# Kernel optimization log

Hardware: AMD Instinct MI355X
Metric: run time of the kernel (lower is better)

The kernel has to match this reference:

```python
import jax, jax.numpy as jnp
import numpy as np

B, N, IN_DIM = 16, 768, 16
HID, EMB, N_LAYERS, N_HEADS = 64, 128, 2, 8


def setup_inputs() -> dict:
    key = jax.random.key(0)
    ks = jax.random.split(key, 10)
    s = lambda fan_in: 1.0 / np.sqrt(fan_in)
    inp = {
        "x": jax.random.normal(ks[0], (B, N, IN_DIM), dtype=jnp.float32),
        "ip_w": jax.random.uniform(ks[1], (IN_DIM, HID), jnp.float32, -s(IN_DIM), s(IN_DIM)),
        "ip_b": jax.random.uniform(ks[2], (HID,), jnp.float32, -s(IN_DIM), s(IN_DIM)),
        # layer 0: in_features = HID; layer 1: in_features = HID * N_HEADS
        "gat_w0": jax.random.uniform(ks[3], (N_HEADS, HID, HID), jnp.float32, -s(HID), s(HID)),
        "gat_a0": jax.random.uniform(ks[4], (N_HEADS, 2 * HID), jnp.float32, -s(2 * HID), s(2 * HID)),
        "gat_w1": jax.random.uniform(ks[5], (N_HEADS, HID * N_HEADS, HID), jnp.float32, -s(HID * N_HEADS), s(HID * N_HEADS)),
        "gat_a1": jax.random.uniform(ks[6], (N_HEADS, 2 * HID), jnp.float32, -s(2 * HID), s(2 * HID)),
        "proj_w": jax.random.uniform(ks[7], (HID * N_HEADS, EMB), jnp.float32, -s(HID * N_HEADS), s(HID * N_HEADS)),
        "proj_b": jax.random.uniform(ks[8], (EMB,), jnp.float32, -s(HID * N_HEADS), s(HID * N_HEADS)),
    }
    return inp


def _gat_layer(h, W, a):
    # h: [B, N, F_in]; W: [H, F_in, F_out]; a: [H, 2*F_out]
    Wh = jnp.einsum("bnf,hfo->bhno", h, W)  # [B,H,N,F_out]
    f_out = W.shape[-1]
    a1, a2 = a[:, :f_out], a[:, f_out:]
    # additive attention decomposed: e_ij = leakyrelu(a1.Wh_i + a2.Wh_j)
    s1 = jnp.einsum("bhno,ho->bhn", Wh, a1)
    s2 = jnp.einsum("bhno,ho->bhn", Wh, a2)
    e = jax.nn.leaky_relu(s1[..., :, None] + s2[..., None, :], negative_slope=0.2)
    # adj = ones -> mask is a no-op; dense softmax over neighbors
    att = jax.nn.softmax(e, axis=-1)  # [B,H,N,N]
    hp = jnp.einsum("bhnm,bhmo->bhno", att, Wh)
    b, hds, n, f = hp.shape
    return hp.transpose(0, 2, 1, 3).reshape(b, n, hds * f)  # concat heads


def reference(x, ip_w, ip_b, gat_w0, gat_a0, gat_w1, gat_a1, proj_w, proj_b):
    h = x @ ip_w + ip_b  # input_proj
    h = _gat_layer(h, gat_w0, gat_a0)
    h = _gat_layer(h, gat_w1, gat_a1)
    # dropout identity (eval); final activation (ELU) is never applied in forward
    return h @ proj_w + proj_b  # [B, N, EMB]
```

## Files before the change

kernel.cpp:

```cpp
#include <hip/hip_runtime.h>
#include <hip/hip_bf16.h>


#define B_ 16
#define N_ 768
#define IN_DIM_ 16
#define HID_ 64
#define EMB_ 128
#define NH_ 8
#define F1_ (NH_ * HID_)
#define LOG2E_ 1.4426950408889634f

typedef __attribute__((ext_vector_type(4))) float f32x4;
typedef __attribute__((ext_vector_type(8))) short bf16x8;

static __device__ __forceinline__ short f2bf(float x) {
    __hip_bfloat16 b = __float2bfloat16(x);
    return *reinterpret_cast<short*>(&b);
}

__global__ __launch_bounds__(256) void k_h0frag(const float* __restrict__ x,
                                                const float* __restrict__ w,
                                                const float* __restrict__ bias,
                                                ushort* __restrict__ h0A) {
    const int t = blockIdx.x * 256 + threadIdx.x;
    const int lane = t & 63;
    const int kt = (t >> 6) & 1;
    const int rtg = t >> 7;
    const int row = rtg * 16 + (lane & 15);
    const int k0 = kt * 32 + (lane >> 4) * 8;
    const float* xr = x + row * IN_DIM_;
    float xv[IN_DIM_];
#pragma unroll
    for (int f = 0; f < IN_DIM_; ++f) xv[f] = xr[f];
    bf16x8 v;
#pragma unroll
    for (int j = 0; j < 8; ++j) {
        float acc = bias[k0 + j];
#pragma unroll
        for (int f = 0; f < IN_DIM_; ++f) acc = fmaf(xv[f], w[f * HID_ + k0 + j], acc);
        v[j] = f2bf(acc);
    }
    *(bf16x8*)&h0A[t * 8] = v;
}

__global__ __launch_bounds__(256) void k_cvtw(const float* __restrict__ w1,
                                              const float* __restrict__ pw,
                                              const float* __restrict__ w0,
                                              ushort* __restrict__ W1f,
                                              ushort* __restrict__ pwf,
                                              ushort* __restrict__ W0f) {
    int t = blockIdx.x * 256 + threadIdx.x;
    if (t < 32768) {
        int lane = t & 63, nt = (t >> 6) & 3, kt = (t >> 8) & 15, h = t >> 12;
        int k0 = kt * 32 + (lane >> 4) * 8;
        int col = nt * 16 + (lane & 15);
        const float* src = w1 + (h * 512 + k0) * 64 + col;
        bf16x8 v;
#pragma unroll
        for (int j = 0; j < 8; ++j) v[j] = f2bf(src[j * 64]);
        *(bf16x8*)&W1f[t * 8] = v;
    } else if (t < 40960) {
        int u = t - 32768;
        int lane = u & 63, nt = (u >> 6) & 7, kt = u >> 9;
        int k0 = kt * 32 + (lane >> 4) * 8;
        int col = nt * 16 + (lane & 15);
        const float* src = pw + k0 * 128 + col;
        bf16x8 v;
#pragma unroll
        for (int j = 0; j < 8; ++j) v[j] = f2bf(src[j * 128]);
        *(bf16x8*)&pwf[u * 8] = v;
    } else {
        int u = t - 40960;
        int lane = u & 63, nt = (u >> 6) & 3, kt = (u >> 8) & 1, h = u >> 9;
        int k0 = kt * 32 + (lane >> 4) * 8;
        int col = nt * 16 + (lane & 15);
        const float* src = w0 + (h * 64 + k0) * 64 + col;
        bf16x8 v;
#pragma unroll
        for (int j = 0; j < 8; ++j) v[j] = f2bf(src[j * 64]);
        *(bf16x8*)&W0f[u * 8] = v;
    }
}

#define TBSTRIDE 40

__global__ __launch_bounds__(256) void k_wh1m(const ushort* __restrict__ h0A,
                                              const ushort* __restrict__ W0f,
                                              const float* __restrict__ a,
                                              ushort* __restrict__ Whf,
                                              float* __restrict__ s1,
                                              float* __restrict__ s2) {
    __shared__ __align__(16) ushort tb[4][64 * TBSTRIDE];
    const int bid = blockIdx.x;
    const int chunk = bid % 6;
    const int h = (bid / 6) % NH_;
    const int b = bid / (6 * NH_);
    const int bh = b * NH_ + h;

    const int lane = threadIdx.x & 63;
    const int w = threadIdx.x >> 6;
    const int lg = lane >> 4;
    const int ll = lane & 15;

    f32x4 zero4 = {0.f, 0.f, 0.f, 0.f};
    f32x4 acc[2][4];
#pragma unroll
    for (int mt = 0; mt < 2; ++mt)
#pragma unroll
        for (int nt = 0; nt < 4; ++nt) acc[mt][nt] = zero4;

    const int rt0 = b * 48 + chunk * 8 + w * 2;
#pragma unroll
    for (int kt = 0; kt < 2; ++kt) {
        bf16x8 afr[2];
#pragma unroll
        for (int mt = 0; mt < 2; ++mt)
            afr[mt] = *(const bf16x8*)&h0A[(((rt0 + mt) * 2) + kt) * 512 + lane * 8];
        bf16x8 bfr[4];
#pragma unroll
        for (int nt = 0; nt < 4; ++nt)
            bfr[nt] = *(const bf16x8*)&W0f[(((h * 2 + kt) * 4) + nt) * 512 + lane * 8];
#pragma unroll
        for (int mt = 0; mt < 2; ++mt)
#pragma unroll
            for (int nt = 0; nt < 4; ++nt)
                acc[mt][nt] = __builtin_amdgcn_mfma_f32_16x16x32_bf16(afr[mt], bfr[nt], acc[mt][nt], 0, 0, 0);
    }

    float a1v[4], a2v[4];
#pragma unroll
    for (int nt = 0; nt < 4; ++nt) {
        a1v[nt] = a[h * 2 * HID_ + nt * 16 + ll];
        a2v[nt] = a[h * 2 * HID_ + HID_ + nt * 16 + ll];
    }
    const int n0 = chunk * 128;
    float* s1b = s1 + bh * N_ + n0 + w * 32;
    float* s2b = s2 + bh * N_ + n0 + w * 32;
    ushort* tbw = tb[w];
#pragma unroll
    for (int mt = 0; mt < 2; ++mt) {
#pragma unroll
        for (int reg = 0; reg < 4; ++reg) {
            const int r32 = mt * 16 + lg * 4 + reg;
            float p1 = 0.f, p2 = 0.f;
#pragma unroll
            for (int nt = 0; nt < 4; ++nt) {
                float v = acc[mt][nt][reg];
                p1 = fmaf(v, a1v[nt], p1);
                p2 = fmaf(v, a2v[nt], p2);
            }
#pragma unroll
            for (int off = 8; off; off >>= 1) {
                p1 += __shfl_xor(p1, off);
                p2 += __shfl_xor(p2, off);
            }
            if (ll == 0) {
                s1b[r32] = p1;
                s2b[r32] = p2;
            }
#pragma unroll
            for (int nt = 0; nt < 4; ++nt) {
                int c = nt * 16 + ll;
                tbw[c * TBSTRIDE + r32] = (ushort)f2bf(acc[mt][nt][reg]);
            }
        }
    }
    __syncthreads();

    const int kt2 = chunk * 4 + w;
#pragma unroll
    for (int nt = 0; nt < 4; ++nt) {
        int c = nt * 16 + ll;
        bf16x8 v = *(const bf16x8*)&tbw[c * TBSTRIDE + lg * 8];
        *(bf16x8*)&Whf[(bh * 24 + kt2) * 2048 + nt * 512 + lane * 8] = v;
    }
}

__global__ __launch_bounds__(256) void k_attn(const ushort* __restrict__ Whf,
                                              const float* __restrict__ s1,
                                              const float* __restrict__ s2,
                                              ushort* __restrict__ hpA) {
    __shared__ __align__(16) float t1s[128];
    __shared__ __align__(16) float t2s[N_];
    __shared__ __align__(16) float dls[128];
    __shared__ __align__(16) ushort hbuf[128 * 64];
    const int bid = blockIdx.x;
    const int nc = bid % (N_ / 128);
    const int h = (bid / (N_ / 128)) % NH_;
    const int b = bid / ((N_ / 128) * NH_);
    const int n0 = nc * 128;
    const int bh = b * NH_ + h;

    const float* s1g = s1 + bh * N_;
    const float* s2g = s2 + bh * N_;
    for (int i = threadIdx.x; i < N_; i += 256) t2s[i] = s2g[i] * LOG2E_;
    if (threadIdx.x < 128) t1s[threadIdx.x] = s1g[n0 + threadIdx.x] * LOG2E_;
    __syncthreads();

    const int lane = threadIdx.x & 63;
    const int w = threadIdx.x >> 6;
    const int rowbase = w * 32;
    const int lg = lane >> 4;
    const int ll = lane & 15;

    const float t1a = t1s[rowbase + ll];
    const float t1b = t1s[rowbase + 16 + ll];

    f32x4 zero4 = {0.f, 0.f, 0.f, 0.f};
    f32x4 acc[2][4];
    f32x4 dacc[2];
#pragma unroll
    for (int mt = 0; mt < 2; ++mt) {
        dacc[mt] = zero4;
#pragma unroll
        for (int nt = 0; nt < 4; ++nt) acc[mt][nt] = zero4;
    }

    bf16x8 onesB;
#pragma unroll
    for (int j = 0; j < 8; ++j) onesB[j] = (ll == 0) ? (short)0x3F80 : (short)0;

    const ushort* Wbase = Whf + bh * ((N_ / 32) * 2048);

    for (int ktile = 0; ktile < N_ / 32; ++ktile) {
        bf16x8 bq[4];
        const ushort* p = Wbase + ktile * 2048 + lane * 8;
#pragma unroll
        for (int nt = 0; nt < 4; ++nt) bq[nt] = *(const bf16x8*)(p + nt * 512);

        float qv[8];
        const float* q = &t2s[ktile * 32 + lg * 8];
#pragma unroll
        for (int j = 0; j < 8; ++j) qv[j] = q[j];

#pragma unroll
        for (int mt = 0; mt < 2; ++mt) {
            const float t1v = mt ? t1b : t1a;
            bf16x8 af;
#pragma unroll
            for (int j = 0; j < 8; ++j) {
                float e = t1v + qv[j];
                e = fmaxf(e, 0.2f * e);
                af[j] = f2bf(exp2f(e));
            }
            dacc[mt] = __builtin_amdgcn_mfma_f32_16x16x32_bf16(af, onesB, dacc[mt], 0, 0, 0);
#pragma unroll
            for (int nt = 0; nt < 4; ++nt)
                acc[mt][nt] = __builtin_amdgcn_mfma_f32_16x16x32_bf16(af, bq[nt], acc[mt][nt], 0, 0, 0);
        }
    }

#pragma unroll
    for (int mt = 0; mt < 2; ++mt) {
        if (ll == 0) {
#pragma unroll
            for (int reg = 0; reg < 4; ++reg)
                dls[rowbase + mt * 16 + lg * 4 + reg] = dacc[mt][reg];
        }
    }
    __syncthreads();

    char* hb8 = (char*)hbuf;
#pragma unroll
    for (int mt = 0; mt < 2; ++mt) {
#pragma unroll
        for (int reg = 0; reg < 4; ++reg) {
            const int row = rowbase + mt * 16 + lg * 4 + reg;
            const float inv = 1.0f / dls[row];
            const int swz = (row & 7) << 4;
#pragma unroll
            for (int nt = 0; nt < 4; ++nt) {
                int c = nt * 16 + ll;
                *(ushort*)(hb8 + row * 128 + ((c * 2) ^ swz)) =
                    (ushort)f2bf(acc[mt][nt][reg] * inv);
            }
        }
    }
    __syncthreads();

#pragma unroll
    for (int rt2 = 0; rt2 < 2; ++rt2) {
#pragma unroll
        for (int kc = 0; kc < 2; ++kc) {
            const int rtl = w * 2 + rt2;
            const int row = rtl * 16 + ll;
            bf16x8 v = *(const bf16x8*)(hb8 + row * 128 +
                                        (((kc * 64 + lg * 16)) ^ ((row & 7) << 4)));
            const int rtg = b * 48 + nc * 8 + rtl;
            *(bf16x8*)&hpA[((rtg * 16) + (h * 2 + kc)) * 512 + lane * 8] = v;
        }
    }
}

__global__ __launch_bounds__(256) void k_wh2(const ushort* __restrict__ hpA,
                                             const ushort* __restrict__ W1f,
                                             const float* __restrict__ a,
                                             ushort* __restrict__ Whf,
                                             float* __restrict__ s1,
                                             float* __restrict__ s2) {
    __shared__ __align__(16) ushort tb[4][64 * TBSTRIDE];
    const int bid = blockIdx.x;
    const int chunk = bid % 6;
    const int h = (bid / 6) % NH_;
    const int b = bid / (6 * NH_);
    const int bh = b * NH_ + h;

    const int lane = threadIdx.x & 63;
    const int w = threadIdx.x >> 6;
    const int lg = lane >> 4;
    const int ll = lane & 15;

    f32x4 zero4 = {0.f, 0.f, 0.f, 0.f};
    f32x4 acc[2][4];
#pragma unroll
    for (int mt = 0; mt < 2; ++mt)
#pragma unroll
        for (int nt = 0; nt < 4; ++nt) acc[mt][nt] = zero4;

    const int rt0 = b * 48 + chunk * 8 + w * 2;
    for (int kt = 0; kt < 16; ++kt) {
        bf16x8 afr[2];
#pragma unroll
        for (int mt = 0; mt < 2; ++mt)
            afr[mt] = *(const bf16x8*)&hpA[(((rt0 + mt) * 16) + kt) * 512 + lane * 8];
        bf16x8 bfr[4];
#pragma unroll
        for (int nt = 0; nt < 4; ++nt)
            bfr[nt] = *(const bf16x8*)&W1f[(((h * 16 + kt) * 4) + nt) * 512 + lane * 8];
#pragma unroll
        for (int mt = 0; mt < 2; ++mt)
#pragma unroll
            for (int nt = 0; nt < 4; ++nt)
                acc[mt][nt] = __builtin_amdgcn_mfma_f32_16x16x32_bf16(afr[mt], bfr[nt], acc[mt][nt], 0, 0, 0);
    }

    float a1v[4], a2v[4];
#pragma unroll
    for (int nt = 0; nt < 4; ++nt) {
        a1v[nt] = a[h * 2 * HID_ + nt * 16 + ll];
        a2v[nt] = a[h * 2 * HID_ + HID_ + nt * 16 + ll];
    }
    const int n0 = chunk * 128;
    float* s1b = s1 + bh * N_ + n0 + w * 32;
    float* s2b = s2 + bh * N_ + n0 + w * 32;
    ushort* tbw = tb[w];
#pragma unroll
    for (int mt = 0; mt < 2; ++mt) {
#pragma unroll
        for (int reg = 0; reg < 4; ++reg) {
            const int r32 = mt * 16 + lg * 4 + reg;
            float p1 = 0.f, p2 = 0.f;
#pragma unroll
            for (int nt = 0; nt < 4; ++nt) {
                float v = acc[mt][nt][reg];
                p1 = fmaf(v, a1v[nt], p1);
                p2 = fmaf(v, a2v[nt], p2);
            }
#pragma unroll
            for (int off = 8; off; off >>= 1) {
                p1 += __shfl_xor(p1, off);
                p2 += __shfl_xor(p2, off);
            }
            if (ll == 0) {
                s1b[r32] = p1;
                s2b[r32] = p2;
            }
#pragma unroll
            for (int nt = 0; nt < 4; ++nt) {
                int c = nt * 16 + ll;
                tbw[c * TBSTRIDE + r32] = (ushort)f2bf(acc[mt][nt][reg]);
            }
        }
    }
    __syncthreads();

    const int kt2 = chunk * 4 + w;
#pragma unroll
    for (int nt = 0; nt < 4; ++nt) {
        int c = nt * 16 + ll;
        bf16x8 v = *(const bf16x8*)&tbw[c * TBSTRIDE + lg * 8];
        *(bf16x8*)&Whf[(bh * 24 + kt2) * 2048 + nt * 512 + lane * 8] = v;
    }
}

__global__ __launch_bounds__(256) void k_projm(const ushort* __restrict__ hpA,
                                               const ushort* __restrict__ pwf,
                                               const float* __restrict__ bias,
                                               float* __restrict__ out) {
    const int blk = blockIdx.x;
    const int lane = threadIdx.x & 63;
    const int w = threadIdx.x >> 6;
    const int wrow = w >> 1, wcol = w & 1;
    const int lg = lane >> 4;
    const int ll = lane & 15;

    f32x4 zero4 = {0.f, 0.f, 0.f, 0.f};
    f32x4 acc[4];
#pragma unroll
    for (int nt = 0; nt < 4; ++nt) acc[nt] = zero4;

    const int rt = blk * 2 + wrow;
    for (int kt = 0; kt < 16; ++kt) {
        bf16x8 afr = *(const bf16x8*)&hpA[((rt * 16) + kt) * 512 + lane * 8];
        bf16x8 bfr[4];
#pragma unroll
        for (int nt = 0; nt < 4; ++nt)
            bfr[nt] = *(const bf16x8*)&pwf[((kt * 8) + wcol * 4 + nt) * 512 + lane * 8];
#pragma unroll
        for (int nt = 0; nt < 4; ++nt)
            acc[nt] = __builtin_amdgcn_mfma_f32_16x16x32_bf16(afr, bfr[nt], acc[nt], 0, 0, 0);
    }

#pragma unroll
    for (int reg = 0; reg < 4; ++reg) {
        const int row = blk * 32 + wrow * 16 + lg * 4 + reg;
#pragma unroll
        for (int nt = 0; nt < 4; ++nt) {
            const int col = wcol * 64 + nt * 16 + ll;
            out[row * EMB_ + col] = acc[nt][reg] + bias[col];
        }
    }
}

extern "C" void kernel_launch(void* const* d_in, const int* in_sizes, int n_in,
                              void* d_out, int out_size, void* d_ws, size_t ws_size,
                              hipStream_t stream) {
    const float* x    = (const float*)d_in[0];
    const float* ip_w = (const float*)d_in[1];
    const float* ip_b = (const float*)d_in[2];
    const float* gw0  = (const float*)d_in[3];
    const float* ga0  = (const float*)d_in[4];
    const float* gw1  = (const float*)d_in[5];
    const float* ga1  = (const float*)d_in[6];
    const float* pw   = (const float*)d_in[7];
    const float* pb   = (const float*)d_in[8];
    float* out = (float*)d_out;

    ushort* h0A = (ushort*)d_ws;
    ushort* Whf = h0A + 786432;
    float* s1 = (float*)(Whf + 6291456);
    float* s2 = s1 + B_ * NH_ * N_;
    ushort* hpA = (ushort*)(s2 + B_ * NH_ * N_);
    ushort* W1f = hpA + 6291456;
    ushort* pwf = W1f + 262144;
    ushort* W0f = pwf + 65536;

    const int attn_blocks = B_ * NH_ * (N_ / 128);
    const int wh_blocks = B_ * NH_ * 6;

    k_cvtw<<<176, 256, 0, stream>>>(gw1, pw, gw0, W1f, pwf, W0f);
    k_h0frag<<<384, 256, 0, stream>>>(x, ip_w, ip_b, h0A);
    k_wh1m<<<wh_blocks, 256, 0, stream>>>(h0A, W0f, ga0, Whf, s1, s2);
    k_attn<<<attn_blocks, 256, 0, stream>>>(Whf, s1, s2, hpA);
    k_wh2<<<wh_blocks, 256, 0, stream>>>(hpA, W1f, ga1, Whf, s1, s2);
    k_attn<<<attn_blocks, 256, 0, stream>>>(Whf, s1, s2, hpA);
    k_projm<<<(B_ * N_) / 32, 256, 0, stream>>>(hpA, pwf, pb, out);
}
```

Before: 171.6 us.

## Double-buffer B operands via direct global-to-LDS loads and fuse prep kernels

Merges the input-projection and weight-conversion kernels into one launch. Adds a double-buffered LDS staging path using global_load_lds in the attention, layer-2 Wh and projection kernels, prefetching the next K-tile while MFMAs run on the current one. Also remaps block indices so heads vary fastest across blocks. In exchange it adds a __syncthreads per K-iteration and extra LDS use, which could lower occupancy or add stalls.

```diff
diff --git a/kernel.cpp b/kernel.cpp
--- a/kernel.cpp
+++ b/kernel.cpp
@@ -14,43 +14,51 @@
 typedef __attribute__((ext_vector_type(4))) float f32x4;
 typedef __attribute__((ext_vector_type(8))) short bf16x8;
 
+typedef __attribute__((address_space(1))) const unsigned int gu32;
+typedef __attribute__((address_space(3))) unsigned int lu32;
+
+static __device__ __forceinline__ void gload_lds16(const void* g, void* l) {
+    __builtin_amdgcn_global_load_lds((gu32*)g, (lu32*)l, 16, 0, 0);
+}
+
 static __device__ __forceinline__ short f2bf(float x) {
     __hip_bfloat16 b = __float2bfloat16(x);
     return *reinterpret_cast<short*>(&b);
 }
 
-__global__ __launch_bounds__(256) void k_h0frag(const float* __restrict__ x,
-                                                const float* __restrict__ w,
-                                                const float* __restrict__ bias,
-                                                ushort* __restrict__ h0A) {
-    const int t = blockIdx.x * 256 + threadIdx.x;
-    const int lane = t & 63;
-    const int kt = (t >> 6) & 1;
-    const int rtg = t >> 7;
-    const int row = rtg * 16 + (lane & 15);
-    const int k0 = kt * 32 + (lane >> 4) * 8;
-    const float* xr = x + row * IN_DIM_;
-    float xv[IN_DIM_];
-#pragma unroll
-    for (int f = 0; f < IN_DIM_; ++f) xv[f] = xr[f];
-    bf16x8 v;
-#pragma unroll
-    for (int j = 0; j < 8; ++j) {
-        float acc = bias[k0 + j];
-#pragma unroll
-        for (int f = 0; f < IN_DIM_; ++f) acc = fmaf(xv[f], w[f * HID_ + k0 + j], acc);
-        v[j] = f2bf(acc);
-    }
-    *(bf16x8*)&h0A[t * 8] = v;
-}
-
-__global__ __launch_bounds__(256) void k_cvtw(const float* __restrict__ w1,
+__global__ __launch_bounds__(256) void k_prep(const float* __restrict__ x,
+                                              const float* __restrict__ ipw,
+                                              const float* __restrict__ ipb,
+                                              const float* __restrict__ w1,
                                               const float* __restrict__ pw,
                                               const float* __restrict__ w0,
+                                              ushort* __restrict__ h0A,
                                               ushort* __restrict__ W1f,
                                               ushort* __restrict__ pwf,
                                               ushort* __restrict__ W0f) {
-    int t = blockIdx.x * 256 + threadIdx.x;
+    if (blockIdx.x < 384) {
+        const int t = blockIdx.x * 256 + threadIdx.x;
+        const int lane = t & 63;
+        const int kt = (t >> 6) & 1;
+        const int rtg = t >> 7;
+        const int row = rtg * 16 + (lane & 15);
+        const int k0 = kt * 32 + (lane >> 4) * 8;
+        const float* xr = x + row * IN_DIM_;
+        float xv[IN_DIM_];
+#pragma unroll
+        for (int f = 0; f < IN_DIM_; ++f) xv[f] = xr[f];
+        bf16x8 v;
+#pragma unroll
+        for (int j = 0; j < 8; ++j) {
+            float acc = ipb[k0 + j];
+#pragma unroll
+            for (int f = 0; f < IN_DIM_; ++f) acc = fmaf(xv[f], ipw[f * HID_ + k0 + j], acc);
+            v[j] = f2bf(acc);
+        }
+        *(bf16x8*)&h0A[t * 8] = v;
+        return;
+    }
+    int t = (blockIdx.x - 384) * 256 + threadIdx.x;
     if (t < 32768) {
         int lane = t & 63, nt = (t >> 6) & 3, kt = (t >> 8) & 15, h = t >> 12;
         int k0 = kt * 32 + (lane >> 4) * 8;
@@ -93,9 +101,10 @@
                                               float* __restrict__ s2) {
     __shared__ __align__(16) ushort tb[4][64 * TBSTRIDE];
     const int bid = blockIdx.x;
-    const int chunk = bid % 6;
-    const int h = (bid / 6) % NH_;
-    const int b = bid / (6 * NH_);
+    const int h = bid & 7;
+    const int rest = bid >> 3;
+    const int b = rest & 15;
+    const int chunk = rest >> 4;
     const int bh = b * NH_ + h;
 
     const int lane = threadIdx.x & 63;
@@ -185,28 +194,30 @@
     __shared__ __align__(16) float t2s[N_];
     __shared__ __align__(16) float dls[128];
     __shared__ __align__(16) ushort hbuf[128 * 64];
+    __shared__ __align__(16) ushort sbuf[2][2048];
     const int bid = blockIdx.x;
-    const int nc = bid % (N_ / 128);
-    const int h = (bid / (N_ / 128)) % NH_;
-    const int b = bid / ((N_ / 128) * NH_);
+    const int h = bid & 7;
+    const int rest = bid >> 3;
+    const int b = rest & 15;
+    const int nc = rest >> 4;
     const int n0 = nc * 128;
     const int bh = b * NH_ + h;
+
+    const int lane = threadIdx.x & 63;
+    const int w = threadIdx.x >> 6;
 
     const float* s1g = s1 + bh * N_;
     const float* s2g = s2 + bh * N_;
     for (int i = threadIdx.x; i < N_; i += 256) t2s[i] = s2g[i] * LOG2E_;
     if (threadIdx.x < 128) t1s[threadIdx.x] = s1g[n0 + threadIdx.x] * LOG2E_;
-    __syncthreads();
-
-    const int lane = threadIdx.x & 63;
-    const int w = threadIdx.x >> 6;
+
+    const ushort* Wbase = Whf + bh * ((N_ / 32) * 2048);
+    gload_lds16(Wbase + threadIdx.x * 8, &sbuf[0][w * 512]);
+
     const int rowbase = w * 32;
     const int lg = lane >> 4;
     const int ll = lane & 15;
 
-    const float t1a = t1s[rowbase + ll];
-    const float t1b = t1s[rowbase + 16 + ll];
-
     f32x4 zero4 = {0.f, 0.f, 0.f, 0.f};
     f32x4 acc[2][4];
     f32x4 dacc[2];
@@ -221,13 +232,21 @@
 #pragma unroll
     for (int j = 0; j < 8; ++j) onesB[j] = (ll == 0) ? (short)0x3F80 : (short)0;
 
-    const ushort* Wbase = Whf + bh * ((N_ / 32) * 2048);
-
+    float t1a = 0.f, t1b = 0.f;
+    int cur = 0;
     for (int ktile = 0; ktile < N_ / 32; ++ktile) {
+        __syncthreads();
+        if (ktile == 0) {
+            t1a = t1s[rowbase + ll];
+            t1b = t1s[rowbase + 16 + ll];
+        }
+        if (ktile + 1 < N_ / 32)
+            gload_lds16(Wbase + (ktile + 1) * 2048 + threadIdx.x * 8, &sbuf[cur ^ 1][w * 512]);
+
+        const ushort* sb = sbuf[cur];
         bf16x8 bq[4];
-        const ushort* p = Wbase + ktile * 2048 + lane * 8;
-#pragma unroll
-        for (int nt = 0; nt < 4; ++nt) bq[nt] = *(const bf16x8*)(p + nt * 512);
+#pragma unroll
+        for (int nt = 0; nt < 4; ++nt) bq[nt] = *(const bf16x8*)&sb[nt * 512 + lane * 8];
 
         float qv[8];
         const float* q = &t2s[ktile * 32 + lg * 8];
@@ -249,6 +268,7 @@
             for (int nt = 0; nt < 4; ++nt)
                 acc[mt][nt] = __builtin_amdgcn_mfma_f32_16x16x32_bf16(af, bq[nt], acc[mt][nt], 0, 0, 0);
         }
+        cur ^= 1;
     }
 
 #pragma unroll
@@ -300,10 +320,12 @@
                                              float* __restrict__ s1,
                                              float* __restrict__ s2) {
     __shared__ __align__(16) ushort tb[4][64 * TBSTRIDE];
+    __shared__ __align__(16) ushort sbuf[2][2048];
     const int bid = blockIdx.x;
-    const int chunk = bid % 6;
-    const int h = (bid / 6) % NH_;
-    const int b = bid / (6 * NH_);
+    const int h = bid & 7;
+    const int rest = bid >> 3;
+    const int b = rest & 15;
+    const int chunk = rest >> 4;
     const int bh = b * NH_ + h;
 
     const int lane = threadIdx.x & 63;
@@ -318,21 +340,30 @@
 #pragma unroll
         for (int nt = 0; nt < 4; ++nt) acc[mt][nt] = zero4;
 
+    const ushort* W1base = W1f + h * 16 * 2048;
+    gload_lds16(W1base + threadIdx.x * 8, &sbuf[0][w * 512]);
+
     const int rt0 = b * 48 + chunk * 8 + w * 2;
+    int cur = 0;
     for (int kt = 0; kt < 16; ++kt) {
+        __syncthreads();
+        if (kt + 1 < 16)
+            gload_lds16(W1base + (kt + 1) * 2048 + threadIdx.x * 8, &sbuf[cur ^ 1][w * 512]);
         bf16x8 afr[2];
 #pragma unroll
         for (int mt = 0; mt < 2; ++mt)
             afr[mt] = *(const bf16x8*)&hpA[(((rt0 + mt) * 16) + kt) * 512 + lane * 8];
+        const ushort* sb = sbuf[cur];
         bf16x8 bfr[4];
 #pragma unroll
         for (int nt = 0; nt < 4; ++nt)
-            bfr[nt] = *(const bf16x8*)&W1f[(((h * 16 + kt) * 4) + nt) * 512 + lane * 8];
+            bfr[nt] = *(const bf16x8*)&sb[nt * 512 + lane * 8];
 #pragma unroll
         for (int mt = 0; mt < 2; ++mt)
 #pragma unroll
             for (int nt = 0; nt < 4; ++nt)
                 acc[mt][nt] = __builtin_amdgcn_mfma_f32_16x16x32_bf16(afr[mt], bfr[nt], acc[mt][nt], 0, 0, 0);
+        cur ^= 1;
     }
 
     float a1v[4], a2v[4];
@@ -388,6 +419,7 @@
                                                const ushort* __restrict__ pwf,
                                                const float* __restrict__ bias,
                                                float* __restrict__ out) {
+    __shared__ __align__(16) ushort sbuf[2][4096];
     const int blk = blockIdx.x;
     const int lane = threadIdx.x & 63;
     const int w = threadIdx.x >> 6;
@@ -400,16 +432,28 @@
 #pragma unroll
     for (int nt = 0; nt < 4; ++nt) acc[nt] = zero4;
 
+    gload_lds16(pwf + threadIdx.x * 8, &sbuf[0][w * 512]);
+    gload_lds16(pwf + 2048 + threadIdx.x * 8, &sbuf[0][2048 + w * 512]);
+
     const int rt = blk * 2 + wrow;
+    int cur = 0;
     for (int kt = 0; kt < 16; ++kt) {
+        __syncthreads();
+        if (kt + 1 < 16) {
+            const ushort* row = pwf + (kt + 1) * 4096;
+            gload_lds16(row + threadIdx.x * 8, &sbuf[cur ^ 1][w * 512]);
+            gload_lds16(row + 2048 + threadIdx.x * 8, &sbuf[cur ^ 1][2048 + w * 512]);
+        }
         bf16x8 afr = *(const bf16x8*)&hpA[((rt * 16) + kt) * 512 + lane * 8];
+        const ushort* sb = sbuf[cur];
         bf16x8 bfr[4];
 #pragma unroll
         for (int nt = 0; nt < 4; ++nt)
-            bfr[nt] = *(const bf16x8*)&pwf[((kt * 8) + wcol * 4 + nt) * 512 + lane * 8];
+            bfr[nt] = *(const bf16x8*)&sb[(wcol * 4 + nt) * 512 + lane * 8];
 #pragma unroll
         for (int nt = 0; nt < 4; ++nt)
             acc[nt] = __builtin_amdgcn_mfma_f32_16x16x32_bf16(afr, bfr[nt], acc[nt], 0, 0, 0);
+        cur ^= 1;
     }
 
 #pragma unroll
@@ -446,14 +490,12 @@
     ushort* pwf = W1f + 262144;
     ushort* W0f = pwf + 65536;
 
-    const int attn_blocks = B_ * NH_ * (N_ / 128);
-    const int wh_blocks = B_ * NH_ * 6;
-
-    k_cvtw<<<176, 256, 0, stream>>>(gw1, pw, gw0, W1f, pwf, W0f);
-    k_h0frag<<<384, 256, 0, stream>>>(x, ip_w, ip_b, h0A);
-    k_wh1m<<<wh_blocks, 256, 0, stream>>>(h0A, W0f, ga0, Whf, s1, s2);
-    k_attn<<<attn_blocks, 256, 0, stream>>>(Whf, s1, s2, hpA);
-    k_wh2<<<wh_blocks, 256, 0, stream>>>(hpA, W1f, ga1, Whf, s1, s2);
-    k_attn<<<attn_blocks, 256, 0, stream>>>(Whf, s1, s2, hpA);
+    const int gat_blocks = 768;
+
+    k_prep<<<560, 256, 0, stream>>>(x, ip_w, ip_b, gw1, pw, gw0, h0A, W1f, pwf, W0f);
+    k_wh1m<<<gat_blocks, 256, 0, stream>>>(h0A, W0f, ga0, Whf, s1, s2);
+    k_attn<<<gat_blocks, 256, 0, stream>>>(Whf, s1, s2, hpA);
+    k_wh2<<<gat_blocks, 256, 0, stream>>>(hpA, W1f, ga1, Whf, s1, s2);
+    k_attn<<<gat_blocks, 256, 0, stream>>>(Whf, s1, s2, hpA);
     k_projm<<<(B_ * N_) / 32, 256, 0, stream>>>(hpA, pwf, pb, out);
 }
```

New measurement: 177.4 us. +3.4%, slower.

## Fuse Wh projection and attention into one per-head GAT kernel

Applied to the files above, without the earlier changes.

Replaces the separate Wh-projection and attention kernels with a single templated k_gat kernel. Each block computes the full Wh for one (batch, head) in LDS and then runs attention over half the query rows, so the Whf and s1/s2 round-trips through global memory go away. The attention scores are computed as an extra MFMA against precomputed W·a vectors (u) instead of a shuffle reduction. Weight prep and input projection are merged into one launch, and layer-1 weights are staged into LDS via global_load_lds. The cost is that each of the two blocks per head recomputes the whole Wh, and the large LDS footprint limits occupancy.

```diff
diff --git a/kernel.cpp b/kernel.cpp
--- a/kernel.cpp
+++ b/kernel.cpp
@@ -8,49 +8,57 @@
 #define HID_ 64
 #define EMB_ 128
 #define NH_ 8
-#define F1_ (NH_ * HID_)
 #define LOG2E_ 1.4426950408889634f
 
 typedef __attribute__((ext_vector_type(4))) float f32x4;
 typedef __attribute__((ext_vector_type(8))) short bf16x8;
+typedef __attribute__((ext_vector_type(4))) short bf16x4;
+
+typedef __attribute__((address_space(1))) const unsigned int gu32;
+typedef __attribute__((address_space(3))) unsigned int lu32;
+
+static __device__ __forceinline__ void gload_lds16(const void* g, void* l) {
+    __builtin_amdgcn_global_load_lds((gu32*)g, (lu32*)l, 16, 0, 0);
+}
 
 static __device__ __forceinline__ short f2bf(float x) {
     __hip_bfloat16 b = __float2bfloat16(x);
     return *reinterpret_cast<short*>(&b);
 }
 
-__global__ __launch_bounds__(256) void k_h0frag(const float* __restrict__ x,
-                                                const float* __restrict__ w,
-                                                const float* __restrict__ bias,
-                                                ushort* __restrict__ h0A) {
-    const int t = blockIdx.x * 256 + threadIdx.x;
-    const int lane = t & 63;
-    const int kt = (t >> 6) & 1;
-    const int rtg = t >> 7;
-    const int row = rtg * 16 + (lane & 15);
-    const int k0 = kt * 32 + (lane >> 4) * 8;
-    const float* xr = x + row * IN_DIM_;
-    float xv[IN_DIM_];
-#pragma unroll
-    for (int f = 0; f < IN_DIM_; ++f) xv[f] = xr[f];
-    bf16x8 v;
-#pragma unroll
-    for (int j = 0; j < 8; ++j) {
-        float acc = bias[k0 + j];
-#pragma unroll
-        for (int f = 0; f < IN_DIM_; ++f) acc = fmaf(xv[f], w[f * HID_ + k0 + j], acc);
-        v[j] = f2bf(acc);
-    }
-    *(bf16x8*)&h0A[t * 8] = v;
-}
-
-__global__ __launch_bounds__(256) void k_cvtw(const float* __restrict__ w1,
+__global__ __launch_bounds__(256) void k_prep(const float* __restrict__ x,
+                                              const float* __restrict__ ipw,
+                                              const float* __restrict__ ipb,
+                                              const float* __restrict__ w1,
                                               const float* __restrict__ pw,
                                               const float* __restrict__ w0,
+                                              ushort* __restrict__ h0A,
                                               ushort* __restrict__ W1f,
                                               ushort* __restrict__ pwf,
                                               ushort* __restrict__ W0f) {
-    int t = blockIdx.x * 256 + threadIdx.x;
+    if (blockIdx.x < 384) {
+        const int t = blockIdx.x * 256 + threadIdx.x;
+        const int lane = t & 63;
+        const int kt = (t >> 6) & 1;
+        const int rtg = t >> 7;
+        const int row = rtg * 16 + (lane & 15);
+        const int k0 = kt * 32 + (lane >> 4) * 8;
+        const float* xr = x + row * IN_DIM_;
+        float xv[IN_DIM_];
+#pragma unroll
+        for (int f = 0; f < IN_DIM_; ++f) xv[f] = xr[f];
+        bf16x8 v;
+#pragma unroll
+        for (int j = 0; j < 8; ++j) {
+            float acc = ipb[k0 + j];
+#pragma unroll
+            for (int f = 0; f < IN_DIM_; ++f) acc = fmaf(xv[f], ipw[f * HID_ + k0 + j], acc);
+            v[j] = f2bf(acc);
+        }
+        *(bf16x8*)&h0A[t * 8] = v;
+        return;
+    }
+    int t = (blockIdx.x - 384) * 256 + threadIdx.x;
     if (t < 32768) {
         int lane = t & 63, nt = (t >> 6) & 3, kt = (t >> 8) & 15, h = t >> 12;
         int k0 = kt * 32 + (lane >> 4) * 8;
@@ -70,7 +78,7 @@
 #pragma unroll
         for (int j = 0; j < 8; ++j) v[j] = f2bf(src[j * 128]);
         *(bf16x8*)&pwf[u * 8] = v;
-    } else {
+    } else if (t < 45056) {
         int u = t - 40960;
         int lane = u & 63, nt = (u >> 6) & 3, kt = (u >> 8) & 1, h = u >> 9;
         int k0 = kt * 32 + (lane >> 4) * 8;
@@ -83,304 +91,205 @@
     }
 }
 
-#define TBSTRIDE 40
-
-__global__ __launch_bounds__(256) void k_wh1m(const ushort* __restrict__ h0A,
-                                              const ushort* __restrict__ W0f,
-                                              const float* __restrict__ a,
-                                              ushort* __restrict__ Whf,
-                                              float* __restrict__ s1,
-                                              float* __restrict__ s2) {
-    __shared__ __align__(16) ushort tb[4][64 * TBSTRIDE];
+__global__ __launch_bounds__(256) void k_ufrag(const float* __restrict__ w1,
+                                               const float* __restrict__ a1g,
+                                               const float* __restrict__ w0,
+                                               const float* __restrict__ a0g,
+                                               float* __restrict__ u1s,
+                                               float* __restrict__ u0s) {
     const int bid = blockIdx.x;
-    const int chunk = bid % 6;
-    const int h = (bid / 6) % NH_;
-    const int b = bid / (6 * NH_);
-    const int bh = b * NH_ + h;
-
-    const int lane = threadIdx.x & 63;
-    const int w = threadIdx.x >> 6;
+    const int tid = threadIdx.x;
+    const int kl = tid >> 3;
+    const int og = tid & 7;
+    const float* W;
+    const float* A;
+    float* U;
+    if (bid < 256) {
+        int sel = bid & 1, kt = (bid >> 1) & 15, h = bid >> 5;
+        W = w1 + (h * 512 + kt * 32 + kl) * 64;
+        A = a1g + h * 128 + sel * 64;
+        U = u1s + (h * 2 + sel) * 512 + kt * 32 + kl;
+    } else {
+        int u = bid - 256;
+        int sel = u & 1, kt = (u >> 1) & 1, h = u >> 2;
+        W = w0 + (h * 64 + kt * 32 + kl) * 64;
+        A = a0g + h * 128 + sel * 64;
+        U = u0s + (h * 2 + sel) * 64 + kt * 32 + kl;
+    }
+    float4 w0v = *(const float4*)&W[og * 8];
+    float4 w1v = *(const float4*)&W[og * 8 + 4];
+    float4 a0v = *(const float4*)&A[og * 8];
+    float4 a1v = *(const float4*)&A[og * 8 + 4];
+    float r = w0v.x * a0v.x + w0v.y * a0v.y + w0v.z * a0v.z + w0v.w * a0v.w +
+              w1v.x * a1v.x + w1v.y * a1v.y + w1v.z * a1v.z + w1v.w * a1v.w;
+    r += __shfl_xor(r, 1);
+    r += __shfl_xor(r, 2);
+    r += __shfl_xor(r, 4);
+    if (og == 0) *U = r * LOG2E_;
+}
+
+template <int KT>
+__global__ __launch_bounds__(512, 2) void k_gat(const ushort* __restrict__ Afrag,
+                                                const ushort* __restrict__ Bfrag,
+                                                const float* __restrict__ us,
+                                                ushort* __restrict__ hpA) {
+    __shared__ __align__(16) char smem[98304];
+    __shared__ __align__(16) float s1s[N_];
+    __shared__ __align__(16) float s2s[N_];
+    ushort* whf = (ushort*)smem;
+
+    const int bid = blockIdx.x;
+    const int half = bid & 1;
+    const int h = (bid >> 1) & 7;
+    const int b = bid >> 4;
+
+    const int tid = threadIdx.x;
+    const int lane = tid & 63;
+    const int w = tid >> 6;
     const int lg = lane >> 4;
     const int ll = lane & 15;
 
-    f32x4 zero4 = {0.f, 0.f, 0.f, 0.f};
-    f32x4 acc[2][4];
-#pragma unroll
-    for (int mt = 0; mt < 2; ++mt)
-#pragma unroll
-        for (int nt = 0; nt < 4; ++nt) acc[mt][nt] = zero4;
-
-    const int rt0 = b * 48 + chunk * 8 + w * 2;
-#pragma unroll
-    for (int kt = 0; kt < 2; ++kt) {
-        bf16x8 afr[2];
-#pragma unroll
-        for (int mt = 0; mt < 2; ++mt)
-            afr[mt] = *(const bf16x8*)&h0A[(((rt0 + mt) * 2) + kt) * 512 + lane * 8];
+    if constexpr (KT == 16) {
+        const ushort* src = Bfrag + h * 16 * 2048;
+#pragma unroll
+        for (int r = 0; r < 8; ++r)
+            gload_lds16(src + r * 4096 + tid * 8, (char*)smem + r * 8192 + w * 1024);
+        __syncthreads();
+    }
+
+    f32x4 acc[6][4];
+    f32x4 accs[6];
+#pragma unroll
+    for (int i = 0; i < 6; ++i) {
+        accs[i] = (f32x4){0.f, 0.f, 0.f, 0.f};
+#pragma unroll
+        for (int nt = 0; nt < 4; ++nt) acc[i][nt] = (f32x4){0.f, 0.f, 0.f, 0.f};
+    }
+
+    for (int kt = 0; kt < KT; ++kt) {
         bf16x8 bfr[4];
+        if constexpr (KT == 16) {
+#pragma unroll
+            for (int nt = 0; nt < 4; ++nt)
+                bfr[nt] = *(const bf16x8*)&whf[kt * 2048 + nt * 512 + lane * 8];
+        } else {
+#pragma unroll
+            for (int nt = 0; nt < 4; ++nt)
+                bfr[nt] = *(const bf16x8*)&Bfrag[((h * 2 + kt) * 4 + nt) * 512 + lane * 8];
+        }
+        bf16x8 ufr = {0, 0, 0, 0, 0, 0, 0, 0};
+        if (ll < 2) {
+            const float* uq = us + (h * 2 + ll) * (KT * 32) + kt * 32 + lg * 8;
+            float4 a0 = *(const float4*)uq;
+            float4 a1 = *(const float4*)(uq + 4);
+            ufr[0] = f2bf(a0.x); ufr[1] = f2bf(a0.y); ufr[2] = f2bf(a0.z); ufr[3] = f2bf(a0.w);
+            ufr[4] = f2bf(a1.x); ufr[5] = f2bf(a1.y); ufr[6] = f2bf(a1.z); ufr[7] = f2bf(a1.w);
+        }
+#pragma unroll
+        for (int i = 0; i < 6; ++i) {
+            const int rt = w * 6 + i;
+            bf16x8 afr = *(const bf16x8*)&Afrag[((b * 48 + rt) * KT + kt) * 512 + lane * 8];
+#pragma unroll
+            for (int nt = 0; nt < 4; ++nt)
+                acc[i][nt] = __builtin_amdgcn_mfma_f32_16x16x32_bf16(afr, bfr[nt], acc[i][nt], 0, 0, 0);
+            accs[i] = __builtin_amdgcn_mfma_f32_16x16x32_bf16(afr, ufr, accs[i], 0, 0, 0);
+        }
+    }
+    if constexpr (KT == 16) __syncthreads();
+
+#pragma unroll
+    for (int i = 0; i < 6; ++i) {
+        const int rt = w * 6 + i;
+        const int lp = ((rt * 2 + (lg >> 1)) & 3) * 16 + ll;
+        const int j0 = 4 * (lg & 1);
+#pragma unroll
+        for (int nt = 0; nt < 4; ++nt) {
+            bf16x4 pk;
+#pragma unroll
+            for (int reg = 0; reg < 4; ++reg) pk[reg] = f2bf(acc[i][nt][reg]);
+            *(bf16x4*)&whf[(((rt >> 1) * 4 + nt) * 64 + lp) * 8 + j0] = pk;
+        }
+#pragma unroll
+        for (int reg = 0; reg < 4; ++reg) {
+            const int row = rt * 16 + lg * 4 + reg;
+            if (ll == 0) s1s[row] = accs[i][reg];
+            else if (ll == 1) s2s[row] = accs[i][reg];
+        }
+    }
+    __syncthreads();
+
+    const int qbase = half * 384 + w * 48;
+    float t1v[3];
+#pragma unroll
+    for (int mt = 0; mt < 3; ++mt) t1v[mt] = s1s[qbase + mt * 16 + ll];
+
+    f32x4 pacc[3][4];
+    f32x4 dacc[3];
+#pragma unroll
+    for (int mt = 0; mt < 3; ++mt) {
+        dacc[mt] = (f32x4){0.f, 0.f, 0.f, 0.f};
+#pragma unroll
+        for (int nt = 0; nt < 4; ++nt) pacc[mt][nt] = (f32x4){0.f, 0.f, 0.f, 0.f};
+    }
+    bf16x8 onesB;
+#pragma unroll
+    for (int j = 0; j < 8; ++j) onesB[j] = (ll == 0) ? (short)0x3F80 : (short)0;
+
+    for (int kt = 0; kt < 24; ++kt) {
+        bf16x8 bq[4];
 #pragma unroll
         for (int nt = 0; nt < 4; ++nt)
-            bfr[nt] = *(const bf16x8*)&W0f[(((h * 2 + kt) * 4) + nt) * 512 + lane * 8];
-#pragma unroll
-        for (int mt = 0; mt < 2; ++mt)
-#pragma unroll
-            for (int nt = 0; nt < 4; ++nt)
-                acc[mt][nt] = __builtin_amdgcn_mfma_f32_16x16x32_bf16(afr[mt], bfr[nt], acc[mt][nt], 0, 0, 0);
-    }
-
-    float a1v[4], a2v[4];
-#pragma unroll
-    for (int nt = 0; nt < 4; ++nt) {
-        a1v[nt] = a[h * 2 * HID_ + nt * 16 + ll];
-        a2v[nt] = a[h * 2 * HID_ + HID_ + nt * 16 + ll];
-    }
-    const int n0 = chunk * 128;
-    float* s1b = s1 + bh * N_ + n0 + w * 32;
-    float* s2b = s2 + bh * N_ + n0 + w * 32;
-    ushort* tbw = tb[w];
-#pragma unroll
-    for (int mt = 0; mt < 2; ++mt) {
-#pragma unroll
-        for (int reg = 0; reg < 4; ++reg) {
-            const int r32 = mt * 16 + lg * 4 + reg;
-            float p1 = 0.f, p2 = 0.f;
-#pragma unroll
-            for (int nt = 0; nt < 4; ++nt) {
-                float v = acc[mt][nt][reg];
-                p1 = fmaf(v, a1v[nt], p1);
-                p2 = fmaf(v, a2v[nt], p2);
-            }
-#pragma unroll
-            for (int off = 8; off; off >>= 1) {
-                p1 += __shfl_xor(p1, off);
-                p2 += __shfl_xor(p2, off);
-            }
-            if (ll == 0) {
-                s1b[r32] = p1;
-                s2b[r32] = p2;
-            }
-#pragma unroll
-            for (int nt = 0; nt < 4; ++nt) {
-                int c = nt * 16 + ll;
-                tbw[c * TBSTRIDE + r32] = (ushort)f2bf(acc[mt][nt][reg]);
-            }
-        }
-    }
-    __syncthreads();
-
-    const int kt2 = chunk * 4 + w;
-#pragma unroll
-    for (int nt = 0; nt < 4; ++nt) {
-        int c = nt * 16 + ll;
-        bf16x8 v = *(const bf16x8*)&tbw[c * TBSTRIDE + lg * 8];
-        *(bf16x8*)&Whf[(bh * 24 + kt2) * 2048 + nt * 512 + lane * 8] = v;
-    }
-}
-
-__global__ __launch_bounds__(256) void k_attn(const ushort* __restrict__ Whf,
-                                              const float* __restrict__ s1,
-                                              const float* __restrict__ s2,
-                                              ushort* __restrict__ hpA) {
-    __shared__ __align__(16) float t1s[128];
-    __shared__ __align__(16) float t2s[N_];
-    __shared__ __align__(16) float dls[128];
-    __shared__ __align__(16) ushort hbuf[128 * 64];
-    const int bid = blockIdx.x;
-    const int nc = bid % (N_ / 128);
-    const int h = (bid / (N_ / 128)) % NH_;
-    const int b = bid / ((N_ / 128) * NH_);
-    const int n0 = nc * 128;
-    const int bh = b * NH_ + h;
-
-    const float* s1g = s1 + bh * N_;
-    const float* s2g = s2 + bh * N_;
-    for (int i = threadIdx.x; i < N_; i += 256) t2s[i] = s2g[i] * LOG2E_;
-    if (threadIdx.x < 128) t1s[threadIdx.x] = s1g[n0 + threadIdx.x] * LOG2E_;
-    __syncthreads();
-
-    const int lane = threadIdx.x & 63;
-    const int w = threadIdx.x >> 6;
-    const int rowbase = w * 32;
-    const int lg = lane >> 4;
-    const int ll = lane & 15;
-
-    const float t1a = t1s[rowbase + ll];
-    const float t1b = t1s[rowbase + 16 + ll];
-
-    f32x4 zero4 = {0.f, 0.f, 0.f, 0.f};
-    f32x4 acc[2][4];
-    f32x4 dacc[2];
-#pragma unroll
-    for (int mt = 0; mt < 2; ++mt) {
-        dacc[mt] = zero4;
-#pragma unroll
-        for (int nt = 0; nt < 4; ++nt) acc[mt][nt] = zero4;
-    }
-
-    bf16x8 onesB;
-#pragma unroll
-    for (int j = 0; j < 8; ++j) onesB[j] = (ll == 0) ? (short)0x3F80 : (short)0;
-
-    const ushort* Wbase = Whf + bh * ((N_ / 32) * 2048);
-
-    for (int ktile = 0; ktile < N_ / 32; ++ktile) {
-        bf16x8 bq[4];
-        const ushort* p = Wbase + ktile * 2048 + lane * 8;
-#pragma unroll
-        for (int nt = 0; nt < 4; ++nt) bq[nt] = *(const bf16x8*)(p + nt * 512);
-
-        float qv[8];
-        const float* q = &t2s[ktile * 32 + lg * 8];
-#pragma unroll
-        for (int j = 0; j < 8; ++j) qv[j] = q[j];
-
-#pragma unroll
-        for (int mt = 0; mt < 2; ++mt) {
-            const float t1v = mt ? t1b : t1a;
+            bq[nt] = *(const bf16x8*)&whf[kt * 2048 + nt * 512 + lane * 8];
+        const float4 q0 = *(const float4*)&s2s[kt * 32 + lg * 8];
+        const float4 q1 = *(const float4*)&s2s[kt * 32 + lg * 8 + 4];
+        float qv[8] = {q0.x, q0.y, q0.z, q0.w, q1.x, q1.y, q1.z, q1.w};
+#pragma unroll
+        for (int mt = 0; mt < 3; ++mt) {
             bf16x8 af;
 #pragma unroll
             for (int j = 0; j < 8; ++j) {
-                float e = t1v + qv[j];
+                float e = t1v[mt] + qv[j];
                 e = fmaxf(e, 0.2f * e);
                 af[j] = f2bf(exp2f(e));
             }
             dacc[mt] = __builtin_amdgcn_mfma_f32_16x16x32_bf16(af, onesB, dacc[mt], 0, 0, 0);
 #pragma unroll
             for (int nt = 0; nt < 4; ++nt)
-                acc[mt][nt] = __builtin_amdgcn_mfma_f32_16x16x32_bf16(af, bq[nt], acc[mt][nt], 0, 0, 0);
-        }
-    }
-
-#pragma unroll
-    for (int mt = 0; mt < 2; ++mt) {
-        if (ll == 0) {
-#pragma unroll
-            for (int reg = 0; reg < 4; ++reg)
-                dls[rowbase + mt * 16 + lg * 4 + reg] = dacc[mt][reg];
+                pacc[mt][nt] = __builtin_amdgcn_mfma_f32_16x16x32_bf16(af, bq[nt], pacc[mt][nt], 0, 0, 0);
         }
     }
     __syncthreads();
 
-    char* hb8 = (char*)hbuf;
-#pragma unroll
-    for (int mt = 0; mt < 2; ++mt) {
+    char* hb8 = smem;
+#pragma unroll
+    for (int mt = 0; mt < 3; ++mt) {
 #pragma unroll
         for (int reg = 0; reg < 4; ++reg) {
-            const int row = rowbase + mt * 16 + lg * 4 + reg;
-            const float inv = 1.0f / dls[row];
-            const int swz = (row & 7) << 4;
+            const int rl = w * 48 + mt * 16 + lg * 4 + reg;
+            const float dv = __shfl(dacc[mt][reg], lane & 0x30);
+            const float inv = 1.0f / dv;
+            const int swz = (rl & 7) << 4;
 #pragma unroll
             for (int nt = 0; nt < 4; ++nt) {
                 int c = nt * 16 + ll;
-                *(ushort*)(hb8 + row * 128 + ((c * 2) ^ swz)) =
-                    (ushort)f2bf(acc[mt][nt][reg] * inv);
+                *(ushort*)(hb8 + rl * 128 + ((c * 2) ^ swz)) =
+                    (ushort)f2bf(pacc[mt][nt][reg] * inv);
             }
         }
     }
     __syncthreads();
 
 #pragma unroll
-    for (int rt2 = 0; rt2 < 2; ++rt2) {
+    for (int rt2 = 0; rt2 < 3; ++rt2) {
 #pragma unroll
         for (int kc = 0; kc < 2; ++kc) {
-            const int rtl = w * 2 + rt2;
+            const int rtl = w * 3 + rt2;
             const int row = rtl * 16 + ll;
             bf16x8 v = *(const bf16x8*)(hb8 + row * 128 +
-                                        (((kc * 64 + lg * 16)) ^ ((row & 7) << 4)));
-            const int rtg = b * 48 + nc * 8 + rtl;
+                                        ((kc * 64 + lg * 16) ^ ((row & 7) << 4)));
+            const int rtg = b * 48 + half * 24 + rtl;
             *(bf16x8*)&hpA[((rtg * 16) + (h * 2 + kc)) * 512 + lane * 8] = v;
         }
-    }
-}
-
-__global__ __launch_bounds__(256) void k_wh2(const ushort* __restrict__ hpA,
-                                             const ushort* __restrict__ W1f,
-                                             const float* __restrict__ a,
-                                             ushort* __restrict__ Whf,
-                                             float* __restrict__ s1,
-                                             float* __restrict__ s2) {
-    __shared__ __align__(16) ushort tb[4][64 * TBSTRIDE];
-    const int bid = blockIdx.x;
-    const int chunk = bid % 6;
-    const int h = (bid / 6) % NH_;
-    const int b = bid / (6 * NH_);
-    const int bh = b * NH_ + h;
-
-    const int lane = threadIdx.x & 63;
-    const int w = threadIdx.x >> 6;
-    const int lg = lane >> 4;
-    const int ll = lane & 15;
-
-    f32x4 zero4 = {0.f, 0.f, 0.f, 0.f};
-    f32x4 acc[2][4];
-#pragma unroll
-    for (int mt = 0; mt < 2; ++mt)
-#pragma unroll
-        for (int nt = 0; nt < 4; ++nt) acc[mt][nt] = zero4;
-
-    const int rt0 = b * 48 + chunk * 8 + w * 2;
-    for (int kt = 0; kt < 16; ++kt) {
-        bf16x8 afr[2];
-#pragma unroll
-        for (int mt = 0; mt < 2; ++mt)
-            afr[mt] = *(const bf16x8*)&hpA[(((rt0 + mt) * 16) + kt) * 512 + lane * 8];
-        bf16x8 bfr[4];
-#pragma unroll
-        for (int nt = 0; nt < 4; ++nt)
-            bfr[nt] = *(const bf16x8*)&W1f[(((h * 16 + kt) * 4) + nt) * 512 + lane * 8];
-#pragma unroll
-        for (int mt = 0; mt < 2; ++mt)
-#pragma unroll
-            for (int nt = 0; nt < 4; ++nt)
-                acc[mt][nt] = __builtin_amdgcn_mfma_f32_16x16x32_bf16(afr[mt], bfr[nt], acc[mt][nt], 0, 0, 0);
-    }
-
-    float a1v[4], a2v[4];
-#pragma unroll
-    for (int nt = 0; nt < 4; ++nt) {
-        a1v[nt] = a[h * 2 * HID_ + nt * 16 + ll];
-        a2v[nt] = a[h * 2 * HID_ + HID_ + nt * 16 + ll];
-    }
-    const int n0 = chunk * 128;
-    float* s1b = s1 + bh * N_ + n0 + w * 32;
-    float* s2b = s2 + bh * N_ + n0 + w * 32;
-    ushort* tbw = tb[w];
-#pragma unroll
-    for (int mt = 0; mt < 2; ++mt) {
-#pragma unroll
-        for (int reg = 0; reg < 4; ++reg) {
-            const int r32 = mt * 16 + lg * 4 + reg;
-            float p1 = 0.f, p2 = 0.f;
-#pragma unroll
-            for (int nt = 0; nt < 4; ++nt) {
-                float v = acc[mt][nt][reg];
-                p1 = fmaf(v, a1v[nt], p1);
-                p2 = fmaf(v, a2v[nt], p2);
-            }
-#pragma unroll
-            for (int off = 8; off; off >>= 1) {
-                p1 += __shfl_xor(p1, off);
-                p2 += __shfl_xor(p2, off);
-            }
-            if (ll == 0) {
-                s1b[r32] = p1;
-                s2b[r32] = p2;
-            }
-#pragma unroll
-            for (int nt = 0; nt < 4; ++nt) {
-                int c = nt * 16 + ll;
-                tbw[c * TBSTRIDE + r32] = (ushort)f2bf(acc[mt][nt][reg]);
-            }
-        }
-    }
-    __syncthreads();
-
-    const int kt2 = chunk * 4 + w;
-#pragma unroll
-    for (int nt = 0; nt < 4; ++nt) {
-        int c = nt * 16 + ll;
-        bf16x8 v = *(const bf16x8*)&tbw[c * TBSTRIDE + lg * 8];
-        *(bf16x8*)&Whf[(bh * 24 + kt2) * 2048 + nt * 512 + lane * 8] = v;
     }
 }
 
@@ -395,10 +304,9 @@
     const int lg = lane >> 4;
     const int ll = lane & 15;
 
-    f32x4 zero4 = {0.f, 0.f, 0.f, 0.f};
     f32x4 acc[4];
 #pragma unroll
-    for (int nt = 0; nt < 4; ++nt) acc[nt] = zero4;
+    for (int nt = 0; nt < 4; ++nt) acc[nt] = (f32x4){0.f, 0.f, 0.f, 0.f};
 
     const int rt = blk * 2 + wrow;
     for (int kt = 0; kt < 16; ++kt) {
@@ -437,23 +345,18 @@
     const float* pb   = (const float*)d_in[8];
     float* out = (float*)d_out;
 
-    ushort* h0A = (ushort*)d_ws;
-    ushort* Whf = h0A + 786432;
-    float* s1 = (float*)(Whf + 6291456);
-    float* s2 = s1 + B_ * NH_ * N_;
-    ushort* hpA = (ushort*)(s2 + B_ * NH_ * N_);
-    ushort* W1f = hpA + 6291456;
-    ushort* pwf = W1f + 262144;
-    ushort* W0f = pwf + 65536;
-
-    const int attn_blocks = B_ * NH_ * (N_ / 128);
-    const int wh_blocks = B_ * NH_ * 6;
-
-    k_cvtw<<<176, 256, 0, stream>>>(gw1, pw, gw0, W1f, pwf, W0f);
-    k_h0frag<<<384, 256, 0, stream>>>(x, ip_w, ip_b, h0A);
-    k_wh1m<<<wh_blocks, 256, 0, stream>>>(h0A, W0f, ga0, Whf, s1, s2);
-    k_attn<<<attn_blocks, 256, 0, stream>>>(Whf, s1, s2, hpA);
-    k_wh2<<<wh_blocks, 256, 0, stream>>>(hpA, W1f, ga1, Whf, s1, s2);
-    k_attn<<<attn_blocks, 256, 0, stream>>>(Whf, s1, s2, hpA);
-    k_projm<<<(B_ * N_) / 32, 256, 0, stream>>>(hpA, pwf, pb, out);
-}
+    ushort* h0A  = (ushort*)d_ws;
+    ushort* hpA0 = h0A + 786432;
+    ushort* hpA1 = hpA0 + 6291456;
+    ushort* W1f  = hpA1 + 6291456;
+    ushort* pwf  = W1f + 262144;
+    ushort* W0f  = pwf + 65536;
+    float*  u1s  = (float*)(W0f + 32768);
+    float*  u0s  = u1s + 8192;
+
+    k_prep<<<560, 256, 0, stream>>>(x, ip_w, ip_b, gw1, pw, gw0, h0A, W1f, pwf, W0f);
+    k_ufrag<<<288, 256, 0, stream>>>(gw1, ga1, gw0, ga0, u1s, u0s);
+    k_gat<2><<<256, 512, 0, stream>>>(h0A, W0f, u0s, hpA0);
+    k_gat<16><<<256, 512, 0, stream>>>(hpA0, W1f, u1s, hpA1);
+    k_projm<<<(B_ * N_) / 32, 256, 0, stream>>>(hpA1, pwf, pb, out);
+}
```

Result: slower. 177.1 us (+3.2%).
